# Optimization experiments

Hardware: AMD Instinct MI355X
Metric: run time of the kernel (lower is better)

The kernel has to match this reference:

```python
import jax, jax.numpy as jnp
import numpy as np

N = 50000   # query points
N2 = 50000  # key/value points
C = 128     # n_channels
G = 8       # n_groups
S = 16      # n_samples
CS = C // G # n_share_channels
EPS = 1e-5


def setup_inputs() -> dict:
    key = jax.random.key(0)
    ks = jax.random.split(key, 16)
    std = 0.02
    return {
        "p": jax.random.normal(ks[0], (N, 3), jnp.float32),
        "x": jax.random.normal(ks[1], (N, C), jnp.float32),
        "p2": jax.random.normal(ks[2], (N2, 3), jnp.float32),
        "x2": jax.random.normal(ks[3], (N2, C), jnp.float32),
        "idx": jax.random.randint(ks[4], (N, S), 0, N2, jnp.int32),
        "Wq": jax.random.normal(ks[5], (C, C), jnp.float32) * std,
        "bq": jnp.zeros((C,), jnp.float32),
        "Wk": jax.random.normal(ks[6], (C, C), jnp.float32) * std,
        "bk": jnp.zeros((C,), jnp.float32),
        "Wv": jax.random.normal(ks[7], (C, C), jnp.float32) * std,
        "bv": jnp.zeros((C,), jnp.float32),
        # linear_p: Conv1d(3,3,1) -> BN(3) -> ReLU -> Conv1d(3, 2G, 1)
        "W1": jax.random.normal(ks[8], (3, 3), jnp.float32) * 0.5,
        "b1": jnp.zeros((3,), jnp.float32),
        "bn_gamma": jnp.ones((3,), jnp.float32),
        "bn_beta": jnp.zeros((3,), jnp.float32),
        "bn_mean": jnp.zeros((3,), jnp.float32),
        "bn_var": jnp.ones((3,), jnp.float32),
        "W2": jax.random.normal(ks[9], (2 * G, 3), jnp.float32) * 0.5,
        "b2": jnp.zeros((2 * G,), jnp.float32),
    }


def reference(p, x, p2, x2, idx,
              Wq, bq, Wk, bk, Wv, bv,
              W1, b1, bn_gamma, bn_beta, bn_mean, bn_var, W2, b2):
    n = x.shape[0]
    # Q/K/V projections
    x_q = x @ Wq.T + bq                       # (n, C)
    x_k = (x2 @ Wk.T + bk)[idx]               # (n, S, C)  KNN gather
    x_v = (x2 @ Wv.T + bv)[idx]               # (n, S, C)
    # relative positions
    p_r = p2[idx] - p[:, None, :]             # (n, S, 3)
    # linear_p (pointwise convs == per-neighbor MLP over the 3 coord channels)
    h = p_r @ W1.T + b1
    h = (h - bn_mean) * jax.lax.rsqrt(bn_var + EPS) * bn_gamma + bn_beta
    h = jax.nn.relu(h)
    pe = h @ W2.T + b2                        # (n, S, 2G)
    p_rq, p_rk = jnp.split(pe, 2, axis=-1)    # each (n, S, G)
    # grouped attention
    k4 = x_k.reshape(n, S, G, CS) + p_rk[..., None]
    q4 = x_q.reshape(n, 1, G, CS) + p_rq[..., None]
    logits = jnp.sum(k4 * q4, axis=-1) / np.float32(np.sqrt(CS))  # (n, S, G)
    w = jax.nn.softmax(logits, axis=1)        # softmax over neighbors
    out = jnp.einsum('nsgc,nsg->ngc', x_v.reshape(n, S, G, CS), w)
    return out.reshape(n, C)
```

## Files before the change

kernel.cpp:

```cpp
#include <hip/hip_runtime.h>
#include <hip/hip_bf16.h>

#define NQ   50000
#define NKV  50000
#define CC   128
#define GG   8
#define SS   16
#define CSH  16

typedef short    bf16x8 __attribute__((ext_vector_type(8)));
typedef float    f32x4  __attribute__((ext_vector_type(4)));
typedef unsigned u32x4  __attribute__((ext_vector_type(4)));
typedef unsigned u32x2  __attribute__((ext_vector_type(2)));
typedef int      i32x4  __attribute__((ext_vector_type(4)));

__device__ __forceinline__ float bf_lo(unsigned u){ union{unsigned x; float f;} v; v.x = u << 16;        return v.f; }
__device__ __forceinline__ float bf_hi(unsigned u){ union{unsigned x; float f;} v; v.x = u & 0xffff0000u; return v.f; }
__device__ __forceinline__ unsigned short f2bfu(float f){
    __hip_bfloat16 h = __float2bfloat16(f);
    return *reinterpret_cast<unsigned short*>(&h);
}
__device__ __forceinline__ short f2bfs(float f){
    __hip_bfloat16 h = __float2bfloat16(f);
    return *reinterpret_cast<short*>(&h);
}

__device__ __forceinline__ void load16bf(const __hip_bfloat16* ptr, float* o){
    const u32x4* p4 = reinterpret_cast<const u32x4*>(ptr);
    u32x4 a = p4[0]; u32x4 b = p4[1];
    o[0]=bf_lo(a[0]);  o[1]=bf_hi(a[0]);  o[2]=bf_lo(a[1]);  o[3]=bf_hi(a[1]);
    o[4]=bf_lo(a[2]);  o[5]=bf_hi(a[2]);  o[6]=bf_lo(a[3]);  o[7]=bf_hi(a[3]);
    o[8]=bf_lo(b[0]);  o[9]=bf_hi(b[0]);  o[10]=bf_lo(b[1]); o[11]=bf_hi(b[1]);
    o[12]=bf_lo(b[2]); o[13]=bf_hi(b[2]); o[14]=bf_lo(b[3]); o[15]=bf_hi(b[3]);
}

__device__ __forceinline__ void load16bf_nt(const __hip_bfloat16* ptr, float* o){
    const u32x4* p4 = reinterpret_cast<const u32x4*>(ptr);
    u32x4 a = __builtin_nontemporal_load(p4);
    u32x4 b = __builtin_nontemporal_load(p4 + 1);
    o[0]=bf_lo(a[0]);  o[1]=bf_hi(a[0]);  o[2]=bf_lo(a[1]);  o[3]=bf_hi(a[1]);
    o[4]=bf_lo(a[2]);  o[5]=bf_hi(a[2]);  o[6]=bf_lo(a[3]);  o[7]=bf_hi(a[3]);
    o[8]=bf_lo(b[0]);  o[9]=bf_hi(b[0]);  o[10]=bf_lo(b[1]); o[11]=bf_hi(b[1]);
    o[12]=bf_lo(b[2]); o[13]=bf_hi(b[2]); o[14]=bf_lo(b[3]); o[15]=bf_hi(b[3]);
}

__device__ __forceinline__ bf16x8 cvt8(const float* p){
    const f32x4* q = reinterpret_cast<const f32x4*>(p);
    f32x4 u = q[0], v = q[1];
    bf16x8 r;
    r[0]=f2bfs(u[0]); r[1]=f2bfs(u[1]); r[2]=f2bfs(u[2]); r[3]=f2bfs(u[3]);
    r[4]=f2bfs(v[0]); r[5]=f2bfs(v[1]); r[6]=f2bfs(v[2]); r[7]=f2bfs(v[3]);
    return r;
}

__global__ __launch_bounds__(256) void qkv_gemm(
    const float* __restrict__ x,
    const float* __restrict__ x2,
    const float* __restrict__ Wq, const float* __restrict__ Wk,
    const float* __restrict__ Wv,
    const float* __restrict__ bq, const float* __restrict__ bk,
    const float* __restrict__ bv,
    __hip_bfloat16* __restrict__ Qf,
    __hip_bfloat16* __restrict__ KVf)
{
    __shared__ short lds16[16384];

    const int which = blockIdx.y;
    const float* src;  const float* W;  const float* bias;
    short* dstb; int dstride, hoff;
    if (which == 0)      { src = x;  W = Wq; bias = bq; dstb = (short*)Qf;  dstride = CC;     hoff = 0;  }
    else if (which == 1) { src = x2; W = Wk; bias = bk; dstb = (short*)KVf; dstride = 2 * CC; hoff = 0;  }
    else                 { src = x2; W = Wv; bias = bv; dstb = (short*)KVf; dstride = 2 * CC; hoff = CC; }
    const int nrows = NQ;

    const int tid = threadIdx.x;
    #pragma unroll
    for (int i = 0; i < 8; ++i) {
        const int o   = i * 2048 + tid * 8;
        const bf16x8 v = cvt8(W + o);
        const int row = o >> 7, col = o & 127;
        const int lchunk = (((row >> 4) * 4 + (col >> 5)) << 6)
                         + (((col >> 3) & 3) << 4) + (row & 15);
        *reinterpret_cast<bf16x8*>(&lds16[lchunk * 8]) = v;
    }

    const int wave = tid >> 6;
    const int lane = tid & 63;
    const int r  = lane & 15;
    const int kq = lane >> 4;
    const int base = blockIdx.x * 128 + wave * 32;

    bf16x8 bfrag[2][4];
    #pragma unroll
    for (int mt = 0; mt < 2; ++mt) {
        int row = base + mt * 16 + r;
        if (row >= nrows) row = nrows - 1;
        const float* xr = src + (size_t)row * CC + kq * 8;
        #pragma unroll
        for (int kb = 0; kb < 4; ++kb)
            bfrag[mt][kb] = cvt8(xr + kb * 32);
    }

    __syncthreads();

    #pragma unroll
    for (int t = 0; t < 8; ++t) {
        bf16x8 af[4];
        #pragma unroll
        for (int kb = 0; kb < 4; ++kb)
            af[kb] = *reinterpret_cast<const bf16x8*>(
                &lds16[(((t * 4 + kb) << 6) + lane) * 8]);

        f32x4 acc0 = {0.f,0.f,0.f,0.f}, acc1 = {0.f,0.f,0.f,0.f};
        #pragma unroll
        for (int kb = 0; kb < 4; ++kb) {
            acc0 = __builtin_amdgcn_mfma_f32_16x16x32_bf16(af[kb], bfrag[0][kb], acc0, 0, 0, 0);
            acc1 = __builtin_amdgcn_mfma_f32_16x16x32_bf16(af[kb], bfrag[1][kb], acc1, 0, 0, 0);
        }

        const f32x4 bi = *reinterpret_cast<const f32x4*>(bias + t * 16 + kq * 4);
        #pragma unroll
        for (int mt = 0; mt < 2; ++mt) {
            const int row = base + mt * 16 + r;
            if (row < nrows) {
                const f32x4 a = mt ? acc1 : acc0;
                u32x2 pk;
                pk[0] = (unsigned)f2bfu(a[0] + bi[0]) | ((unsigned)f2bfu(a[1] + bi[1]) << 16);
                pk[1] = (unsigned)f2bfu(a[2] + bi[2]) | ((unsigned)f2bfu(a[3] + bi[3]) << 16);
                __builtin_nontemporal_store(pk, reinterpret_cast<u32x2*>(
                    dstb + (size_t)row * dstride + hoff + t * 16 + kq * 4));
            }
        }
    }
}

__global__ __launch_bounds__(256) void attn_kernel(
    const float* __restrict__ p,
    const float* __restrict__ p2,
    const int*   __restrict__ idx,
    const float* __restrict__ W1,
    const float* __restrict__ b1,
    const float* __restrict__ bn_gamma,
    const float* __restrict__ bn_beta,
    const float* __restrict__ bn_mean,
    const float* __restrict__ bn_var,
    const float* __restrict__ W2,
    const float* __restrict__ b2,
    const __hip_bfloat16* __restrict__ Qf,
    const __hip_bfloat16* __restrict__ KVf,
    float* __restrict__ out)
{
    const int tid = blockIdx.x * 256 + threadIdx.x;
    if (tid >= NQ * GG) return;
    const int n = tid >> 3;
    const int g = tid & 7;

    float fw1[3][3], fb1[3];
    #pragma unroll
    for (int j = 0; j < 3; ++j) {
        const float sc = bn_gamma[j] * rsqrtf(bn_var[j] + 1e-5f);
        #pragma unroll
        for (int k = 0; k < 3; ++k) fw1[j][k] = W1[j*3 + k] * sc;
        fb1[j] = (b1[j] - bn_mean[j]) * sc + bn_beta[j];
    }
    const float w2q0 = W2[g*3+0],     w2q1 = W2[g*3+1],     w2q2 = W2[g*3+2];
    const float w2k0 = W2[(g+8)*3+0], w2k1 = W2[(g+8)*3+1], w2k2 = W2[(g+8)*3+2];
    const float b2q = b2[g], b2k = b2[g+8];

    const float px = p[(size_t)n*3+0];
    const float py = p[(size_t)n*3+1];
    const float pz = p[(size_t)n*3+2];

    int nbr[SS];
    {
        const i32x4* ip = reinterpret_cast<const i32x4*>(idx + (size_t)n * SS);
        i32x4 i0 = __builtin_nontemporal_load(ip);
        i32x4 i1 = __builtin_nontemporal_load(ip + 1);
        i32x4 i2 = __builtin_nontemporal_load(ip + 2);
        i32x4 i3 = __builtin_nontemporal_load(ip + 3);
        nbr[0]=i0[0]; nbr[1]=i0[1]; nbr[2]=i0[2]; nbr[3]=i0[3];
        nbr[4]=i1[0]; nbr[5]=i1[1]; nbr[6]=i1[2]; nbr[7]=i1[3];
        nbr[8]=i2[0]; nbr[9]=i2[1]; nbr[10]=i2[2]; nbr[11]=i2[3];
        nbr[12]=i3[0]; nbr[13]=i3[1]; nbr[14]=i3[2]; nbr[15]=i3[3];
    }

    float q[CSH];
    load16bf_nt(Qf + (size_t)n * CC + g * CSH, q);

    float acc[CSH];
    #pragma unroll
    for (int c = 0; c < CSH; ++c) acc[c] = 0.f;
    float sum = 0.f;
    float m = -3.0e38f;

    #pragma unroll 4
    for (int s = 0; s < SS; ++s) {
        const int i = nbr[s];
        const __hip_bfloat16* kv = KVf + (size_t)i * (2 * CC) + g * CSH;

        float kk[CSH], vv[CSH];
        load16bf(kv, kk);
        load16bf(kv + CC, vv);

        const float rx = p2[(size_t)i*3+0] - px;
        const float ry = p2[(size_t)i*3+1] - py;
        const float rz = p2[(size_t)i*3+2] - pz;
        const float h0 = fmaxf(fw1[0][0]*rx + fw1[0][1]*ry + fw1[0][2]*rz + fb1[0], 0.f);
        const float h1 = fmaxf(fw1[1][0]*rx + fw1[1][1]*ry + fw1[1][2]*rz + fb1[1], 0.f);
        const float h2 = fmaxf(fw1[2][0]*rx + fw1[2][1]*ry + fw1[2][2]*rz + fb1[2], 0.f);
        const float prq = w2q0*h0 + w2q1*h1 + w2q2*h2 + b2q;
        const float prk = w2k0*h0 + w2k1*h1 + w2k2*h2 + b2k;

        float d = 0.f;
        #pragma unroll
        for (int c = 0; c < CSH; ++c) d += (kk[c] + prk) * (q[c] + prq);
        d *= 0.25f;

        const float mnew = fmaxf(m, d);
        const float corr = __expf(m - mnew);
        const float w    = __expf(d - mnew);
        sum = sum * corr + w;
        #pragma unroll
        for (int c = 0; c < CSH; ++c) acc[c] = acc[c] * corr + w * vv[c];
        m = mnew;
    }

    const float inv = 1.f / sum;

    f32x4* op = reinterpret_cast<f32x4*>(out + (size_t)n * CC + g * CSH);
    f32x4 o0 = {acc[0]*inv,  acc[1]*inv,  acc[2]*inv,  acc[3]*inv};
    f32x4 o1 = {acc[4]*inv,  acc[5]*inv,  acc[6]*inv,  acc[7]*inv};
    f32x4 o2 = {acc[8]*inv,  acc[9]*inv,  acc[10]*inv, acc[11]*inv};
    f32x4 o3 = {acc[12]*inv, acc[13]*inv, acc[14]*inv, acc[15]*inv};
    __builtin_nontemporal_store(o0, op);
    __builtin_nontemporal_store(o1, op + 1);
    __builtin_nontemporal_store(o2, op + 2);
    __builtin_nontemporal_store(o3, op + 3);
}

extern "C" void kernel_launch(void* const* d_in, const int* in_sizes, int n_in,
                              void* d_out, int out_size, void* d_ws, size_t ws_size,
                              hipStream_t stream) {
    const float* p   = (const float*)d_in[0];
    const float* x   = (const float*)d_in[1];
    const float* p2  = (const float*)d_in[2];
    const float* x2  = (const float*)d_in[3];
    const int*   idx = (const int*)d_in[4];
    const float* Wq  = (const float*)d_in[5];
    const float* bq  = (const float*)d_in[6];
    const float* Wk  = (const float*)d_in[7];
    const float* bk  = (const float*)d_in[8];
    const float* Wv  = (const float*)d_in[9];
    const float* bv  = (const float*)d_in[10];
    const float* W1  = (const float*)d_in[11];
    const float* b1  = (const float*)d_in[12];
    const float* bng = (const float*)d_in[13];
    const float* bnb = (const float*)d_in[14];
    const float* bnm = (const float*)d_in[15];
    const float* bnv = (const float*)d_in[16];
    const float* W2  = (const float*)d_in[17];
    const float* b2  = (const float*)d_in[18];
    float* out = (float*)d_out;

    __hip_bfloat16* Qf  = (__hip_bfloat16*)d_ws;
    __hip_bfloat16* KVf = Qf + (size_t)NQ * CC;

    qkv_gemm<<<dim3(391, 3), 256, 0, stream>>>(
        x, x2, Wq, Wk, Wv, bq, bk, bv, Qf, KVf);

    const int nthreads = NQ * GG;
    attn_kernel<<<(nthreads + 255) / 256, 256, 0, stream>>>(
        p, p2, idx, W1, b1, bng, bnb, bnm, bnv, W2, b2, Qf, KVf, out);
}
```

Measured before the change: 230.1 us.

## Share x2 fragments for K and V GEMM, batch neighbor gathers in attention

The QKV GEMM now runs two y-blocks instead of three: the K/V block loads x2 once and reuses its fragments for both the Wk and Wv projections, restaging the weights through LDS between them. The attention kernel processes neighbors in groups of four, issuing all K/V/p2 gathers up front to raise memory-level parallelism. It also rewrites the logit dot product algebraically using precomputed sums of q and k, and does one online-softmax rescale per group of four. Nontemporal loads and stores are replaced with normal ones, and launch bounds request 4 blocks per SM; the larger register footprint from batching could limit occupancy.

```diff
diff --git a/kernel.cpp b/kernel.cpp
--- a/kernel.cpp
+++ b/kernel.cpp
@@ -28,16 +28,6 @@
 __device__ __forceinline__ void load16bf(const __hip_bfloat16* ptr, float* o){
     const u32x4* p4 = reinterpret_cast<const u32x4*>(ptr);
     u32x4 a = p4[0]; u32x4 b = p4[1];
-    o[0]=bf_lo(a[0]);  o[1]=bf_hi(a[0]);  o[2]=bf_lo(a[1]);  o[3]=bf_hi(a[1]);
-    o[4]=bf_lo(a[2]);  o[5]=bf_hi(a[2]);  o[6]=bf_lo(a[3]);  o[7]=bf_hi(a[3]);
-    o[8]=bf_lo(b[0]);  o[9]=bf_hi(b[0]);  o[10]=bf_lo(b[1]); o[11]=bf_hi(b[1]);
-    o[12]=bf_lo(b[2]); o[13]=bf_hi(b[2]); o[14]=bf_lo(b[3]); o[15]=bf_hi(b[3]);
-}
-
-__device__ __forceinline__ void load16bf_nt(const __hip_bfloat16* ptr, float* o){
-    const u32x4* p4 = reinterpret_cast<const u32x4*>(ptr);
-    u32x4 a = __builtin_nontemporal_load(p4);
-    u32x4 b = __builtin_nontemporal_load(p4 + 1);
     o[0]=bf_lo(a[0]);  o[1]=bf_hi(a[0]);  o[2]=bf_lo(a[1]);  o[3]=bf_hi(a[1]);
     o[4]=bf_lo(a[2]);  o[5]=bf_hi(a[2]);  o[6]=bf_lo(a[3]);  o[7]=bf_hi(a[3]);
     o[8]=bf_lo(b[0]);  o[9]=bf_hi(b[0]);  o[10]=bf_lo(b[1]); o[11]=bf_hi(b[1]);
@@ -65,76 +55,90 @@
 {
     __shared__ short lds16[16384];
 
-    const int which = blockIdx.y;
-    const float* src;  const float* W;  const float* bias;
-    short* dstb; int dstride, hoff;
-    if (which == 0)      { src = x;  W = Wq; bias = bq; dstb = (short*)Qf;  dstride = CC;     hoff = 0;  }
-    else if (which == 1) { src = x2; W = Wk; bias = bk; dstb = (short*)KVf; dstride = 2 * CC; hoff = 0;  }
-    else                 { src = x2; W = Wv; bias = bv; dstb = (short*)KVf; dstride = 2 * CC; hoff = CC; }
-    const int nrows = NQ;
-
-    const int tid = threadIdx.x;
-    #pragma unroll
-    for (int i = 0; i < 8; ++i) {
-        const int o   = i * 2048 + tid * 8;
-        const bf16x8 v = cvt8(W + o);
-        const int row = o >> 7, col = o & 127;
-        const int lchunk = (((row >> 4) * 4 + (col >> 5)) << 6)
-                         + (((col >> 3) & 3) << 4) + (row & 15);
-        *reinterpret_cast<bf16x8*>(&lds16[lchunk * 8]) = v;
-    }
-
+    const int tid  = threadIdx.x;
     const int wave = tid >> 6;
     const int lane = tid & 63;
-    const int r  = lane & 15;
-    const int kq = lane >> 4;
+    const int r    = lane & 15;
+    const int kq   = lane >> 4;
     const int base = blockIdx.x * 128 + wave * 32;
 
-    bf16x8 bfrag[2][4];
-    #pragma unroll
-    for (int mt = 0; mt < 2; ++mt) {
-        int row = base + mt * 16 + r;
-        if (row >= nrows) row = nrows - 1;
-        const float* xr = src + (size_t)row * CC + kq * 8;
-        #pragma unroll
-        for (int kb = 0; kb < 4; ++kb)
-            bfrag[mt][kb] = cvt8(xr + kb * 32);
+    auto stageW = [&](const float* __restrict__ W){
+        #pragma unroll
+        for (int i = 0; i < 8; ++i) {
+            const int o   = i * 2048 + tid * 8;
+            const bf16x8 v = cvt8(W + o);
+            const int row = o >> 7, col = o & 127;
+            const int lchunk = (((row >> 4) * 4 + (col >> 5)) << 6)
+                             + (((col >> 3) & 3) << 4) + (row & 15);
+            *reinterpret_cast<bf16x8*>(&lds16[lchunk * 8]) = v;
+        }
+    };
+
+    auto loadB = [&](const float* __restrict__ src, bf16x8 (&bfrag)[2][4]){
+        #pragma unroll
+        for (int mt = 0; mt < 2; ++mt) {
+            int row = base + mt * 16 + r;
+            if (row >= NQ) row = NQ - 1;
+            const float* xr = src + (size_t)row * CC + kq * 8;
+            #pragma unroll
+            for (int kb = 0; kb < 4; ++kb)
+                bfrag[mt][kb] = cvt8(xr + kb * 32);
+        }
+    };
+
+    auto runTiles = [&](const bf16x8 (&bfrag)[2][4], const float* __restrict__ bias,
+                        short* __restrict__ dstb, int dstride, int hoff){
+        #pragma unroll
+        for (int t = 0; t < 8; ++t) {
+            bf16x8 af[4];
+            #pragma unroll
+            for (int kb = 0; kb < 4; ++kb)
+                af[kb] = *reinterpret_cast<const bf16x8*>(
+                    &lds16[(((t * 4 + kb) << 6) + lane) * 8]);
+
+            f32x4 acc0 = {0.f,0.f,0.f,0.f}, acc1 = {0.f,0.f,0.f,0.f};
+            #pragma unroll
+            for (int kb = 0; kb < 4; ++kb) {
+                acc0 = __builtin_amdgcn_mfma_f32_16x16x32_bf16(af[kb], bfrag[0][kb], acc0, 0, 0, 0);
+                acc1 = __builtin_amdgcn_mfma_f32_16x16x32_bf16(af[kb], bfrag[1][kb], acc1, 0, 0, 0);
+            }
+
+            const f32x4 bi = *reinterpret_cast<const f32x4*>(bias + t * 16 + kq * 4);
+            #pragma unroll
+            for (int mt = 0; mt < 2; ++mt) {
+                const int row = base + mt * 16 + r;
+                if (row < NQ) {
+                    const f32x4 a = mt ? acc1 : acc0;
+                    u32x2 pk;
+                    pk[0] = (unsigned)f2bfu(a[0] + bi[0]) | ((unsigned)f2bfu(a[1] + bi[1]) << 16);
+                    pk[1] = (unsigned)f2bfu(a[2] + bi[2]) | ((unsigned)f2bfu(a[3] + bi[3]) << 16);
+                    *reinterpret_cast<u32x2*>(
+                        dstb + (size_t)row * dstride + hoff + t * 16 + kq * 4) = pk;
+                }
+            }
+        }
+    };
+
+    if (blockIdx.y == 0) {
+        bf16x8 bfrag[2][4];
+        loadB(x, bfrag);
+        stageW(Wq);
+        __syncthreads();
+        runTiles(bfrag, bq, (short*)Qf, CC, 0);
+    } else {
+        bf16x8 bfrag[2][4];
+        loadB(x2, bfrag);
+        stageW(Wk);
+        __syncthreads();
+        runTiles(bfrag, bk, (short*)KVf, 2 * CC, 0);
+        __syncthreads();
+        stageW(Wv);
+        __syncthreads();
+        runTiles(bfrag, bv, (short*)KVf, 2 * CC, CC);
     }
-
-    __syncthreads();
-
-    #pragma unroll
-    for (int t = 0; t < 8; ++t) {
-        bf16x8 af[4];
-        #pragma unroll
-        for (int kb = 0; kb < 4; ++kb)
-            af[kb] = *reinterpret_cast<const bf16x8*>(
-                &lds16[(((t * 4 + kb) << 6) + lane) * 8]);
-
-        f32x4 acc0 = {0.f,0.f,0.f,0.f}, acc1 = {0.f,0.f,0.f,0.f};
-        #pragma unroll
-        for (int kb = 0; kb < 4; ++kb) {
-            acc0 = __builtin_amdgcn_mfma_f32_16x16x32_bf16(af[kb], bfrag[0][kb], acc0, 0, 0, 0);
-            acc1 = __builtin_amdgcn_mfma_f32_16x16x32_bf16(af[kb], bfrag[1][kb], acc1, 0, 0, 0);
-        }
-
-        const f32x4 bi = *reinterpret_cast<const f32x4*>(bias + t * 16 + kq * 4);
-        #pragma unroll
-        for (int mt = 0; mt < 2; ++mt) {
-            const int row = base + mt * 16 + r;
-            if (row < nrows) {
-                const f32x4 a = mt ? acc1 : acc0;
-                u32x2 pk;
-                pk[0] = (unsigned)f2bfu(a[0] + bi[0]) | ((unsigned)f2bfu(a[1] + bi[1]) << 16);
-                pk[1] = (unsigned)f2bfu(a[2] + bi[2]) | ((unsigned)f2bfu(a[3] + bi[3]) << 16);
-                __builtin_nontemporal_store(pk, reinterpret_cast<u32x2*>(
-                    dstb + (size_t)row * dstride + hoff + t * 16 + kq * 4));
-            }
-        }
-    }
-}
-
-__global__ __launch_bounds__(256) void attn_kernel(
+}
+
+__global__ __launch_bounds__(256, 4) void attn_kernel(
     const float* __restrict__ p,
     const float* __restrict__ p2,
     const int*   __restrict__ idx,
@@ -171,21 +175,13 @@
     const float py = p[(size_t)n*3+1];
     const float pz = p[(size_t)n*3+2];
 
-    int nbr[SS];
-    {
-        const i32x4* ip = reinterpret_cast<const i32x4*>(idx + (size_t)n * SS);
-        i32x4 i0 = __builtin_nontemporal_load(ip);
-        i32x4 i1 = __builtin_nontemporal_load(ip + 1);
-        i32x4 i2 = __builtin_nontemporal_load(ip + 2);
-        i32x4 i3 = __builtin_nontemporal_load(ip + 3);
-        nbr[0]=i0[0]; nbr[1]=i0[1]; nbr[2]=i0[2]; nbr[3]=i0[3];
-        nbr[4]=i1[0]; nbr[5]=i1[1]; nbr[6]=i1[2]; nbr[7]=i1[3];
-        nbr[8]=i2[0]; nbr[9]=i2[1]; nbr[10]=i2[2]; nbr[11]=i2[3];
-        nbr[12]=i3[0]; nbr[13]=i3[1]; nbr[14]=i3[2]; nbr[15]=i3[3];
-    }
-
     float q[CSH];
-    load16bf_nt(Qf + (size_t)n * CC + g * CSH, q);
+    load16bf(Qf + (size_t)n * CC + g * CSH, q);
+    float Sq = 0.f;
+    #pragma unroll
+    for (int c = 0; c < CSH; ++c) Sq += q[c];
+
+    const i32x4* ip = reinterpret_cast<const i32x4*>(idx + (size_t)n * SS);
 
     float acc[CSH];
     #pragma unroll
@@ -193,36 +189,70 @@
     float sum = 0.f;
     float m = -3.0e38f;
 
-    #pragma unroll 4
-    for (int s = 0; s < SS; ++s) {
-        const int i = nbr[s];
-        const __hip_bfloat16* kv = KVf + (size_t)i * (2 * CC) + g * CSH;
-
-        float kk[CSH], vv[CSH];
-        load16bf(kv, kk);
-        load16bf(kv + CC, vv);
-
-        const float rx = p2[(size_t)i*3+0] - px;
-        const float ry = p2[(size_t)i*3+1] - py;
-        const float rz = p2[(size_t)i*3+2] - pz;
-        const float h0 = fmaxf(fw1[0][0]*rx + fw1[0][1]*ry + fw1[0][2]*rz + fb1[0], 0.f);
-        const float h1 = fmaxf(fw1[1][0]*rx + fw1[1][1]*ry + fw1[1][2]*rz + fb1[1], 0.f);
-        const float h2 = fmaxf(fw1[2][0]*rx + fw1[2][1]*ry + fw1[2][2]*rz + fb1[2], 0.f);
-        const float prq = w2q0*h0 + w2q1*h1 + w2q2*h2 + b2q;
-        const float prk = w2k0*h0 + w2k1*h1 + w2k2*h2 + b2k;
-
-        float d = 0.f;
-        #pragma unroll
-        for (int c = 0; c < CSH; ++c) d += (kk[c] + prk) * (q[c] + prq);
-        d *= 0.25f;
-
-        const float mnew = fmaxf(m, d);
-        const float corr = __expf(m - mnew);
-        const float w    = __expf(d - mnew);
-        sum = sum * corr + w;
-        #pragma unroll
-        for (int c = 0; c < CSH; ++c) acc[c] = acc[c] * corr + w * vv[c];
-        m = mnew;
+    #pragma unroll
+    for (int sc = 0; sc < 4; ++sc) {
+        const i32x4 i4 = ip[sc];
+
+        u32x4 kr[4][2], vr[4][2];
+        float rx[4], ry[4], rz[4];
+        #pragma unroll
+        for (int j = 0; j < 4; ++j) {
+            const int i = i4[j];
+            const u32x4* b = reinterpret_cast<const u32x4*>(
+                KVf + (size_t)i * (2 * CC) + g * CSH);
+            kr[j][0] = b[0];  kr[j][1] = b[1];
+            vr[j][0] = b[16]; vr[j][1] = b[17];
+            rx[j] = p2[(size_t)i*3+0] - px;
+            ry[j] = p2[(size_t)i*3+1] - py;
+            rz[j] = p2[(size_t)i*3+2] - pz;
+        }
+
+        float d[4];
+        #pragma unroll
+        for (int j = 0; j < 4; ++j) {
+            const float h0 = fmaxf(fw1[0][0]*rx[j] + fw1[0][1]*ry[j] + fw1[0][2]*rz[j] + fb1[0], 0.f);
+            const float h1 = fmaxf(fw1[1][0]*rx[j] + fw1[1][1]*ry[j] + fw1[1][2]*rz[j] + fb1[1], 0.f);
+            const float h2 = fmaxf(fw1[2][0]*rx[j] + fw1[2][1]*ry[j] + fw1[2][2]*rz[j] + fb1[2], 0.f);
+            const float prq = w2q0*h0 + w2q1*h1 + w2q2*h2 + b2q;
+            const float prk = w2k0*h0 + w2k1*h1 + w2k2*h2 + b2k;
+
+            float kq = 0.f, Sk = 0.f;
+            #pragma unroll
+            for (int h = 0; h < 2; ++h) {
+                const u32x4 a = kr[j][h];
+                #pragma unroll
+                for (int w4 = 0; w4 < 4; ++w4) {
+                    const float lo = bf_lo(a[w4]), hi = bf_hi(a[w4]);
+                    const int c = h*8 + w4*2;
+                    kq += lo * q[c] + hi * q[c+1];
+                    Sk += lo + hi;
+                }
+            }
+            d[j] = 0.25f * (kq + prq * Sk + prk * Sq + 16.f * prk * prq);
+        }
+
+        const float m4 = fmaxf(fmaxf(fmaxf(d[0], d[1]), fmaxf(d[2], d[3])), m);
+        const float corr = __expf(m - m4);
+        float wj[4];
+        #pragma unroll
+        for (int j = 0; j < 4; ++j) wj[j] = __expf(d[j] - m4);
+        sum = sum * corr + wj[0] + wj[1] + wj[2] + wj[3];
+        #pragma unroll
+        for (int c = 0; c < CSH; ++c) acc[c] *= corr;
+        #pragma unroll
+        for (int j = 0; j < 4; ++j) {
+            #pragma unroll
+            for (int h = 0; h < 2; ++h) {
+                const u32x4 a = vr[j][h];
+                #pragma unroll
+                for (int w4 = 0; w4 < 4; ++w4) {
+                    const int c = h*8 + w4*2;
+                    acc[c]   += wj[j] * bf_lo(a[w4]);
+                    acc[c+1] += wj[j] * bf_hi(a[w4]);
+                }
+            }
+        }
+        m = m4;
     }
 
     const float inv = 1.f / sum;
@@ -232,10 +262,7 @@
     f32x4 o1 = {acc[4]*inv,  acc[5]*inv,  acc[6]*inv,  acc[7]*inv};
     f32x4 o2 = {acc[8]*inv,  acc[9]*inv,  acc[10]*inv, acc[11]*inv};
     f32x4 o3 = {acc[12]*inv, acc[13]*inv, acc[14]*inv, acc[15]*inv};
-    __builtin_nontemporal_store(o0, op);
-    __builtin_nontemporal_store(o1, op + 1);
-    __builtin_nontemporal_store(o2, op + 2);
-    __builtin_nontemporal_store(o3, op + 3);
+    op[0] = o0; op[1] = o1; op[2] = o2; op[3] = o3;
 }
 
 extern "C" void kernel_launch(void* const* d_in, const int* in_sizes, int n_in,
@@ -265,7 +292,7 @@
     __hip_bfloat16* Qf  = (__hip_bfloat16*)d_ws;
     __hip_bfloat16* KVf = Qf + (size_t)NQ * CC;
 
-    qkv_gemm<<<dim3(391, 3), 256, 0, stream>>>(
+    qkv_gemm<<<dim3(391, 2), 256, 0, stream>>>(
         x, x2, Wq, Wk, Wv, bq, bk, bv, Qf, KVf);
 
     const int nthreads = NQ * GG;
```

Result: slower. 608.3 us (+164.3%).
